# Performance work log

Measured on AMD Instinct MI355X. Metric: run time of the kernel, lower is better.

Reference implementation:

```python
import jax, jax.numpy as jnp
import numpy as np
from math import sqrt

B, L, S, H, E, D = 2, 2048, 2048, 16, 64, 64

def setup_inputs() -> dict:
    key = jax.random.key(0)
    kq, kk, kv = jax.random.split(key, 3)
    queries = jax.random.normal(kq, (B, L, H, E), dtype=jnp.float32)
    keys = jax.random.normal(kk, (B, S, H, E), dtype=jnp.float32)
    values = jax.random.normal(kv, (B, S, H, D), dtype=jnp.float32)
    # causal mask: True where attention is NOT allowed (j > i), matching masked_fill_ semantics
    causal = jnp.triu(jnp.ones((L, S), dtype=jnp.bool_), k=1)
    attn_mask = jnp.broadcast_to(causal[None, None, :, :], (B, 1, L, S))
    return {"queries": queries, "keys": keys, "values": values, "attn_mask": attn_mask}

def reference(queries, keys, values, attn_mask):
    # scores: [B,H,L,S]
    scale = 1.0 / sqrt(queries.shape[-1])
    scores = jnp.einsum('blhe,bshe->bhls', queries, keys)
    scores = jnp.where(attn_mask, -jnp.inf, scores)
    A = jax.nn.softmax(scale * scores, axis=-1)
    V = jnp.einsum('bhls,bshd->blhd', A, values)
    return V
```

## Files before the change

kernel.cpp:

```cpp
#include <hip/hip_runtime.h>

typedef unsigned short ushort_t;
typedef __attribute__((ext_vector_type(8))) short s8v;
typedef __attribute__((ext_vector_type(2))) unsigned u2v;
typedef __attribute__((ext_vector_type(4))) unsigned u4v;
typedef __attribute__((ext_vector_type(4))) float f4;

__device__ __forceinline__ ushort_t f2bf(float x) {
    unsigned u = __builtin_bit_cast(unsigned, x);
    return (ushort_t)((u + 0x7FFFu + ((u >> 16) & 1u)) >> 16);
}
__device__ __forceinline__ unsigned pack_hi16(float lo, float hi) {
    unsigned a = __builtin_bit_cast(unsigned, lo);
    unsigned b = __builtin_bit_cast(unsigned, hi);
    return (a >> 16) | (b & 0xFFFF0000u);
}

__global__ __launch_bounds__(256) void prep_kv(const float* __restrict__ K,
                                               const float* __restrict__ V,
                                               ushort_t* __restrict__ Kb,
                                               ushort_t* __restrict__ VT) {
    __shared__ ushort_t T[64 * 72];
    if (blockIdx.x < 2048) {
        const int gid = blockIdx.x * 256 + threadIdx.x;
        const int e = (gid & 7) * 8;
        const int h = (gid >> 3) & 15;
        const int s = (gid >> 7) & 2047;
        const int b = gid >> 18;
        const float* src = K + (((b * 2048 + s) * 16 + h) * 64 + e);
        f4 a = *(const f4*)src;
        f4 c = *(const f4*)(src + 4);
        s8v o;
        #pragma unroll
        for (int j = 0; j < 4; ++j) { o[j] = (short)f2bf(a[j]); o[j + 4] = (short)f2bf(c[j]); }
        *(s8v*)(Kb + (((b * 16 + h) * 2048 + s) * 64 + e)) = o;
    } else {
        const int v = blockIdx.x - 2048;
        const int s0 = (v & 31) * 64;
        const int h  = (v >> 5) & 15;
        const int b  = v >> 9;
        const int t  = threadIdx.x;
        {
            const int srow = t >> 2, dc = (t & 3) * 16;
            const float* src = V + (((b * 2048 + s0 + srow) * 16 + h) * 64 + dc);
            #pragma unroll
            for (int c = 0; c < 4; ++c) {
                f4 vv = *(const f4*)(src + c * 4);
                #pragma unroll
                for (int j = 0; j < 4; ++j) T[(dc + c * 4 + j) * 72 + srow] = f2bf(vv[j]);
            }
        }
        __syncthreads();
        {
            const int d = t >> 2, sq = (t & 3) * 16;
            ushort_t* dst = VT + (((b * 16 + h) * 64 + d) * 2048 + s0 + sq);
            *(s8v*)(dst)     = *(const s8v*)(&T[d * 72 + sq]);
            *(s8v*)(dst + 8) = *(const s8v*)(&T[d * 72 + sq + 8]);
        }
    }
}

__global__ __launch_bounds__(256, 2) void fattn_main(
    const float* __restrict__ Q,
    const ushort_t* __restrict__ Kb,
    const ushort_t* __restrict__ VTb,
    float* __restrict__ O)
{
    constexpr float K1 = 0.18033688011112042f;
    constexpr float SHIFT = 12.0f;
    __shared__ ushort_t KT0[64 * 72];
    __shared__ ushort_t KT1[64 * 72];
    __shared__ ushort_t VT0[64 * 72];
    __shared__ ushort_t VT1[64 * 72];

    const int bx = blockIdx.x;
    const int bh = bx & 31;
    const int p  = bx >> 5;
    const int b = bh >> 4, h = bh & 15;

    const int wave = threadIdx.x >> 6;
    const int lane = threadIdx.x & 63;
    const int l15  = lane & 15;
    const int quad = lane >> 4;

    const ushort_t* kb  = Kb  + bh * (2048 * 64);
    const ushort_t* vtb = VTb + bh * (64 * 2048);
    const float*    qb  = Q + b * (2048 * 1024) + h * 64;
    float*          ob  = O + b * (2048 * 1024) + h * 64;

    const s8v ones = {0x3F80, 0x3F80, 0x3F80, 0x3F80, 0x3F80, 0x3F80, 0x3F80, 0x3F80};
    const f4 zero4 = {0.f, 0.f, 0.f, 0.f};

    const int sr = threadIdx.x >> 2;
    const int sc = (threadIdx.x & 3) << 4;

    int qr0 = p * 64;

    s8v aq[2];
    f4 oacc[4];
    f4 lsum;

    auto loadQ = [&](int qr) {
        const float* qrow = qb + (qr + wave * 16 + l15) * 1024;
        #pragma unroll
        for (int ks = 0; ks < 2; ++ks) {
            f4 x = *(const f4*)(qrow + ks * 32 + quad * 8);
            f4 y = *(const f4*)(qrow + ks * 32 + quad * 8 + 4);
            #pragma unroll
            for (int j = 0; j < 4; ++j) {
                aq[ks][j]     = (short)f2bf(x[j]);
                aq[ks][j + 4] = (short)f2bf(y[j]);
            }
        }
    };
    auto zeroAcc = [&]() {
        lsum = zero4;
        #pragma unroll
        for (int d = 0; d < 4; ++d) oacc[d] = zero4;
    };
    auto storeO = [&](int qr) {
        #pragma unroll
        for (int r = 0; r < 4; ++r) {
            const float inv = 1.0f / lsum[r];
            const int row = qr + wave * 16 + quad * 4 + r;
            #pragma unroll
            for (int dd = 0; dd < 4; ++dd)
                ob[row * 1024 + dd * 16 + l15] = oacc[dd][r] * inv;
        }
    };

    loadQ(qr0);
    zeroAcc();

    {
        const ushort_t* ksrc = kb + sr * 64 + sc;
        const ushort_t* vsrc = vtb + sr * 2048 + sc;
        s8v k0 = *(const s8v*)(ksrc);
        s8v k1 = *(const s8v*)(ksrc + 8);
        s8v v0 = *(const s8v*)(vsrc);
        s8v v1 = *(const s8v*)(vsrc + 8);
        *(s8v*)&KT0[sr * 72 + sc]     = k0;
        *(s8v*)&KT0[sr * 72 + sc + 8] = k1;
        *(s8v*)&VT0[sr * 72 + sc]     = v0;
        *(s8v*)&VT0[sr * 72 + sc + 8] = v1;
    }
    __syncthreads();

    ushort_t* ktr = KT0;  ushort_t* vtr = VT0;
    ushort_t* ktw = KT1;  ushort_t* vtw = VT1;

    for (int n = 0; n < 33; ++n) {
        s8v gK2[2], gV2[2];
        if (n < 32) {
            const int sn = (n + 1 <= p) ? (n + 1) : (n - p);
            const ushort_t* ksrc = kb + (sn * 64 + sr) * 64 + sc;
            const ushort_t* vsrc = vtb + sr * 2048 + sn * 64 + sc;
            gK2[0] = *(const s8v*)(ksrc);    gK2[1] = *(const s8v*)(ksrc + 8);
            gV2[0] = *(const s8v*)(vsrc);    gV2[1] = *(const s8v*)(vsrc + 8);
        }

        const int s_cur = (n <= p) ? n : (n - p - 1);
        const int n0 = s_cur * 64;
        const bool diag = (n == p) || (n == 32);

        f4 st[4];
        __builtin_amdgcn_s_setprio(1);
        #pragma unroll
        for (int t = 0; t < 4; ++t) {
            const s8v bk0 = *(const s8v*)&ktr[(t * 16 + l15) * 72 + quad * 8];
            const s8v bk1 = *(const s8v*)&ktr[(t * 16 + l15) * 72 + 32 + quad * 8];
            f4 a = __builtin_amdgcn_mfma_f32_16x16x32_bf16(bk0, aq[0], zero4, 0, 0, 0);
            st[t] = __builtin_amdgcn_mfma_f32_16x16x32_bf16(bk1, aq[1], a, 0, 0, 0);
        }
        __builtin_amdgcn_s_setprio(0);

        unsigned w[8];
        #pragma unroll
        for (int t = 0; t < 4; ++t) {
            float pv4[4];
            #pragma unroll
            for (int r = 0; r < 4; ++r) {
                float x = __builtin_fmaf(st[t][r], K1, -SHIFT);
                if (diag) {
                    const int gj = n0 + t * 16 + quad * 4 + r;
                    const int gi = qr0 + wave * 16 + l15;
                    if (gj > gi) x = -INFINITY;
                }
                pv4[r] = __builtin_exp2f(x);
            }
            w[t * 2]     = pack_hi16(pv4[0], pv4[1]);
            w[t * 2 + 1] = pack_hi16(pv4[2], pv4[3]);
        }

        asm volatile("v_permlane32_swap_b32 %0, %1" : "+v"(w[0]), "+v"(w[2]));
        asm volatile("v_permlane32_swap_b32 %0, %1" : "+v"(w[1]), "+v"(w[3]));
        asm volatile("v_permlane32_swap_b32 %0, %1" : "+v"(w[4]), "+v"(w[6]));
        asm volatile("v_permlane32_swap_b32 %0, %1" : "+v"(w[5]), "+v"(w[7]));
        asm volatile("v_permlane16_swap_b32 %0, %1" : "+v"(w[0]), "+v"(w[2]));
        asm volatile("v_permlane16_swap_b32 %0, %1" : "+v"(w[1]), "+v"(w[3]));
        asm volatile("v_permlane16_swap_b32 %0, %1" : "+v"(w[4]), "+v"(w[6]));
        asm volatile("v_permlane16_swap_b32 %0, %1" : "+v"(w[5]), "+v"(w[7]));

        u4v a0v = {w[0], w[1], w[2], w[3]};
        u4v a1v = {w[4], w[5], w[6], w[7]};
        const s8v ap0 = __builtin_bit_cast(s8v, a0v);
        const s8v ap1 = __builtin_bit_cast(s8v, a1v);

        #pragma unroll
        for (int ks = 0; ks < 2; ++ks) {
            s8v bvv[4];
            #pragma unroll
            for (int dd = 0; dd < 4; ++dd)
                bvv[dd] = *(const s8v*)&vtr[(dd * 16 + l15) * 72 + ks * 32 + quad * 8];
            const s8v ap = ks ? ap1 : ap0;
            __builtin_amdgcn_s_setprio(1);
            lsum = __builtin_amdgcn_mfma_f32_16x16x32_bf16(ap, ones, lsum, 0, 0, 0);
            #pragma unroll
            for (int dd = 0; dd < 4; ++dd)
                oacc[dd] = __builtin_amdgcn_mfma_f32_16x16x32_bf16(ap, bvv[dd], oacc[dd], 0, 0, 0);
            __builtin_amdgcn_s_setprio(0);
        }

        if (n < 32) {
            *(s8v*)&ktw[sr * 72 + sc]     = gK2[0];
            *(s8v*)&ktw[sr * 72 + sc + 8] = gK2[1];
            *(s8v*)&vtw[sr * 72 + sc]     = gV2[0];
            *(s8v*)&vtw[sr * 72 + sc + 8] = gV2[1];
        }

        __syncthreads();

        { ushort_t* t0 = ktr; ktr = ktw; ktw = t0; }
        { ushort_t* t1 = vtr; vtr = vtw; vtw = t1; }

        if (n == p) {
            storeO(qr0);
            qr0 = (31 - p) * 64;
            loadQ(qr0);
            zeroAcc();
        }
    }

    storeO(qr0);
}

#define PSTR 72
__global__ __launch_bounds__(256) void fattn_fallback(
    const float* __restrict__ Q, const float* __restrict__ K,
    const float* __restrict__ V, float* __restrict__ O)
{
    constexpr int strL = 1024, strB = 2048 * strL;
    const float scale = 0.125f;
    __shared__ ushort_t KT[64 * PSTR];
    __shared__ ushort_t VT[64 * PSTR];
    __shared__ ushort_t P[4][16 * PSTR];
    const int bh = blockIdx.x & 31;
    const int b = bh >> 4, h = bh & 15;
    const int im = 31 - (blockIdx.x >> 5);
    const int q0 = im * 64;
    const int tid = threadIdx.x, wave = tid >> 6, lane = tid & 63;
    const int l15 = lane & 15, quad = lane >> 4;
    const float* qbase = Q + b*strB + (q0 + wave*16 + l15)*strL + h*64;
    s8v aq0, aq1;
    {
        f4 q0v = *(const f4*)(qbase + quad*8);
        f4 q1v = *(const f4*)(qbase + quad*8 + 4);
        f4 q2v = *(const f4*)(qbase + 32 + quad*8);
        f4 q3v = *(const f4*)(qbase + 32 + quad*8 + 4);
        #pragma unroll
        for (int j = 0; j < 4; ++j) {
            aq0[j] = (short)f2bf(q0v[j]); aq0[j+4] = (short)f2bf(q1v[j]);
            aq1[j] = (short)f2bf(q2v[j]); aq1[j+4] = (short)f2bf(q3v[j]);
        }
    }
    const f4 zero4 = {0.f,0.f,0.f,0.f};
    f4 oacc[4]; float m_prev[4], lsum[4];
    #pragma unroll
    for (int d = 0; d < 4; ++d) oacc[d] = zero4;
    #pragma unroll
    for (int r = 0; r < 4; ++r) { m_prev[r] = -INFINITY; lsum[r] = 0.0f; }
    const float* kh = K + b*strB + h*64;
    const float* vh = V + b*strB + h*64;
    for (int it = 0; it <= im; ++it) {
        const int n0 = it * 64;
        __syncthreads();
        {
            const float* krow = kh + (n0 + lane)*strL + wave*16;
            f4 k0 = *(const f4*)(krow); f4 k1 = *(const f4*)(krow+4);
            f4 k2 = *(const f4*)(krow+8); f4 k3 = *(const f4*)(krow+12);
            s8v kb0, kb1;
            #pragma unroll
            for (int j = 0; j < 4; ++j) {
                kb0[j] = (short)f2bf(k0[j]); kb0[j+4] = (short)f2bf(k1[j]);
                kb1[j] = (short)f2bf(k2[j]); kb1[j+4] = (short)f2bf(k3[j]);
            }
            *(s8v*)&KT[lane*PSTR + wave*16] = kb0;
            *(s8v*)&KT[lane*PSTR + wave*16 + 8] = kb1;
            const float* vrow = vh + (n0 + lane)*strL + wave*16;
            f4 v0 = *(const f4*)(vrow); f4 v1 = *(const f4*)(vrow+4);
            f4 v2 = *(const f4*)(vrow+8); f4 v3 = *(const f4*)(vrow+12);
            #pragma unroll
            for (int j = 0; j < 4; ++j) {
                VT[(wave*16 + j)*PSTR + lane] = f2bf(v0[j]);
                VT[(wave*16 + 4 + j)*PSTR + lane] = f2bf(v1[j]);
                VT[(wave*16 + 8 + j)*PSTR + lane] = f2bf(v2[j]);
                VT[(wave*16 + 12 + j)*PSTR + lane] = f2bf(v3[j]);
            }
        }
        __syncthreads();
        f4 sacc[4];
        #pragma unroll
        for (int t = 0; t < 4; ++t) {
            sacc[t] = zero4;
            const s8v bk0 = *(const s8v*)&KT[(t*16 + l15)*PSTR + quad*8];
            const s8v bk1 = *(const s8v*)&KT[(t*16 + l15)*PSTR + 32 + quad*8];
            sacc[t] = __builtin_amdgcn_mfma_f32_16x16x32_bf16(aq0, bk0, sacc[t], 0, 0, 0);
            sacc[t] = __builtin_amdgcn_mfma_f32_16x16x32_bf16(aq1, bk1, sacc[t], 0, 0, 0);
        }
        const bool diag = (it == im);
        float sv[4][4], rmax[4];
        #pragma unroll
        for (int r = 0; r < 4; ++r) rmax[r] = -INFINITY;
        #pragma unroll
        for (int t = 0; t < 4; ++t)
            #pragma unroll
            for (int r = 0; r < 4; ++r) {
                float x = sacc[t][r] * scale;
                if (diag) {
                    const int gi = wave*16 + quad*4 + r;
                    const int gj = t*16 + l15;
                    if (gj > gi) x = -INFINITY;
                }
                sv[t][r] = x; rmax[r] = fmaxf(rmax[r], x);
            }
        #pragma unroll
        for (int off = 8; off >= 1; off >>= 1)
            #pragma unroll
            for (int r = 0; r < 4; ++r)
                rmax[r] = fmaxf(rmax[r], __shfl_xor(rmax[r], off, 64));
        float mnew[4], alpha[4], rsum[4];
        #pragma unroll
        for (int r = 0; r < 4; ++r) {
            mnew[r] = fmaxf(m_prev[r], rmax[r]);
            alpha[r] = __expf(m_prev[r] - mnew[r]);
            m_prev[r] = mnew[r]; rsum[r] = 0.f;
        }
        #pragma unroll
        for (int t = 0; t < 4; ++t)
            #pragma unroll
            for (int r = 0; r < 4; ++r) {
                const float p = __expf(sv[t][r] - mnew[r]);
                rsum[r] += p;
                P[wave][(quad*4 + r)*PSTR + t*16 + l15] = f2bf(p);
            }
        #pragma unroll
        for (int off = 8; off >= 1; off >>= 1)
            #pragma unroll
            for (int r = 0; r < 4; ++r)
                rsum[r] += __shfl_xor(rsum[r], off, 64);
        #pragma unroll
        for (int r = 0; r < 4; ++r) lsum[r] = alpha[r]*lsum[r] + rsum[r];
        #pragma unroll
        for (int d = 0; d < 4; ++d)
            #pragma unroll
            for (int r = 0; r < 4; ++r) oacc[d][r] *= alpha[r];
        #pragma unroll
        for (int ks = 0; ks < 2; ++ks) {
            const s8v ap = *(const s8v*)&P[wave][l15*PSTR + ks*32 + quad*8];
            #pragma unroll
            for (int d = 0; d < 4; ++d) {
                const s8v bvv = *(const s8v*)&VT[(d*16 + l15)*PSTR + ks*32 + quad*8];
                oacc[d] = __builtin_amdgcn_mfma_f32_16x16x32_bf16(ap, bvv, oacc[d], 0, 0, 0);
            }
        }
    }
    float* obase = O + b*strB + h*64;
    #pragma unroll
    for (int r = 0; r < 4; ++r) {
        const float inv = 1.0f / lsum[r];
        const int gi = q0 + wave*16 + quad*4 + r;
        #pragma unroll
        for (int d = 0; d < 4; ++d)
            obase[gi*strL + d*16 + l15] = oacc[d][r] * inv;
    }
}

extern "C" void kernel_launch(void* const* d_in, const int* in_sizes, int n_in,
                              void* d_out, int out_size, void* d_ws, size_t ws_size,
                              hipStream_t stream) {
    const float* Q = (const float*)d_in[0];
    const float* K = (const float*)d_in[1];
    const float* V = (const float*)d_in[2];
    float* O = (float*)d_out;
    const size_t NEED = 2ull * 4194304ull * 2ull;
    if (ws_size >= NEED) {
        ushort_t* Kb = (ushort_t*)d_ws;
        ushort_t* VT = Kb + 4194304;
        prep_kv<<<3072, 256, 0, stream>>>(K, V, Kb, VT);
        fattn_main<<<512, 256, 0, stream>>>(Q, Kb, VT, O);
    } else {
        fattn_fallback<<<1024, 256, 0, stream>>>(Q, K, V, O);
    }
}
```

Measured before the change: 151.1 us.

## Split causal attention work into balanced blocks with partial-sum combine kernel

Adds a split-KV attention kernel launched with 1024 blocks. Each block pairs a short low query tile with half of a long high query tile's key range, so every block does about 16-17 key-tile iterations. Partial unnormalized outputs and row sums for the high tiles are written to workspace, and a new combine kernel adds the two halves and normalizes them. The goal is to remove causal load imbalance and raise occupancy (launch bounds 4). In exchange it adds a third launch and extra global traffic for the partials.

```diff
diff --git a/kernel.cpp b/kernel.cpp
--- a/kernel.cpp
+++ b/kernel.cpp
@@ -57,6 +57,238 @@
             *(s8v*)(dst)     = *(const s8v*)(&T[d * 72 + sq]);
             *(s8v*)(dst + 8) = *(const s8v*)(&T[d * 72 + sq + 8]);
         }
+    }
+}
+
+__global__ __launch_bounds__(256, 4) void fattn_split(
+    const float* __restrict__ Q,
+    const ushort_t* __restrict__ Kb,
+    const ushort_t* __restrict__ VTb,
+    float* __restrict__ O,
+    float* __restrict__ PP)
+{
+    constexpr float K1 = 0.18033688011112042f;
+    constexpr float SHIFT = 12.0f;
+    __shared__ ushort_t KT0[64 * 72];
+    __shared__ ushort_t KT1[64 * 72];
+    __shared__ ushort_t VT0[64 * 72];
+    __shared__ ushort_t VT1[64 * 72];
+
+    const int bx = blockIdx.x;
+    const int bh = bx & 31;
+    const int slot = bx >> 5;
+    const bool roleA = (slot < 16);
+    const int i = roleA ? slot : (slot - 16);
+    const int tHi = 31 - i;
+    const int NIT = roleA ? 17 : 16;
+    const int b = bh >> 4, h = bh & 15;
+
+    const int wave = threadIdx.x >> 6;
+    const int lane = threadIdx.x & 63;
+    const int l15  = lane & 15;
+    const int quad = lane >> 4;
+
+    const ushort_t* kb  = Kb  + bh * (2048 * 64);
+    const ushort_t* vtb = VTb + bh * (64 * 2048);
+    const float*    qb  = Q + b * (2048 * 1024) + h * 64;
+    float*          ob  = O + b * (2048 * 1024) + h * 64;
+
+    const s8v ones = {0x3F80, 0x3F80, 0x3F80, 0x3F80, 0x3F80, 0x3F80, 0x3F80, 0x3F80};
+    const f4 zero4 = {0.f, 0.f, 0.f, 0.f};
+
+    const int sr = threadIdx.x >> 2;
+    const int sc = (threadIdx.x & 3) << 4;
+
+    auto sTileOf = [&](int n) -> int {
+        return roleA ? ((n <= i) ? n : (n - i - 1)) : (16 - i + n);
+    };
+
+    int qr0 = (roleA ? i : tHi) * 64;
+
+    s8v aq[2];
+    f4 oacc[4];
+    f4 lsum;
+
+    auto loadQ = [&](int qr) {
+        const float* qrow = qb + (qr + wave * 16 + l15) * 1024;
+        #pragma unroll
+        for (int ks = 0; ks < 2; ++ks) {
+            f4 x = *(const f4*)(qrow + ks * 32 + quad * 8);
+            f4 y = *(const f4*)(qrow + ks * 32 + quad * 8 + 4);
+            #pragma unroll
+            for (int j = 0; j < 4; ++j) {
+                aq[ks][j]     = (short)f2bf(x[j]);
+                aq[ks][j + 4] = (short)f2bf(y[j]);
+            }
+        }
+    };
+    auto zeroAcc = [&]() {
+        lsum = zero4;
+        #pragma unroll
+        for (int d = 0; d < 4; ++d) oacc[d] = zero4;
+    };
+    auto storeO = [&](int qr) {
+        #pragma unroll
+        for (int r = 0; r < 4; ++r) {
+            const float inv = 1.0f / lsum[r];
+            const int row = qr + wave * 16 + quad * 4 + r;
+            #pragma unroll
+            for (int dd = 0; dd < 4; ++dd)
+                ob[row * 1024 + dd * 16 + l15] = oacc[dd][r] * inv;
+        }
+    };
+    auto storePartial = [&](int side) {
+        float* base = PP + (size_t)(((side * 32 + bh) * 16 + i) * 4160);
+        #pragma unroll
+        for (int r = 0; r < 4; ++r) {
+            const int rl = wave * 16 + quad * 4 + r;
+            #pragma unroll
+            for (int dd = 0; dd < 4; ++dd)
+                base[rl * 64 + dd * 16 + l15] = oacc[dd][r];
+        }
+        if (l15 == 0) {
+            #pragma unroll
+            for (int r = 0; r < 4; ++r)
+                base[4096 + wave * 16 + quad * 4 + r] = lsum[r];
+        }
+    };
+
+    loadQ(qr0);
+    zeroAcc();
+
+    {
+        const int s0 = sTileOf(0);
+        const ushort_t* ksrc = kb + (s0 * 64 + sr) * 64 + sc;
+        const ushort_t* vsrc = vtb + sr * 2048 + s0 * 64 + sc;
+        s8v k0 = *(const s8v*)(ksrc);
+        s8v k1 = *(const s8v*)(ksrc + 8);
+        s8v v0 = *(const s8v*)(vsrc);
+        s8v v1 = *(const s8v*)(vsrc + 8);
+        *(s8v*)&KT0[sr * 72 + sc]     = k0;
+        *(s8v*)&KT0[sr * 72 + sc + 8] = k1;
+        *(s8v*)&VT0[sr * 72 + sc]     = v0;
+        *(s8v*)&VT0[sr * 72 + sc + 8] = v1;
+    }
+    __syncthreads();
+
+    ushort_t* ktr = KT0;  ushort_t* vtr = VT0;
+    ushort_t* ktw = KT1;  ushort_t* vtw = VT1;
+
+    for (int n = 0; n < NIT; ++n) {
+        s8v gK2[2], gV2[2];
+        if (n + 1 < NIT) {
+            const int sn = sTileOf(n + 1);
+            const ushort_t* ksrc = kb + (sn * 64 + sr) * 64 + sc;
+            const ushort_t* vsrc = vtb + sr * 2048 + sn * 64 + sc;
+            gK2[0] = *(const s8v*)(ksrc);    gK2[1] = *(const s8v*)(ksrc + 8);
+            gV2[0] = *(const s8v*)(vsrc);    gV2[1] = *(const s8v*)(vsrc + 8);
+        }
+
+        const int s_cur = sTileOf(n);
+        const int n0 = s_cur * 64;
+        const bool diag = roleA ? (n == i) : (n == 15);
+
+        f4 st[4];
+        __builtin_amdgcn_s_setprio(1);
+        #pragma unroll
+        for (int t = 0; t < 4; ++t) {
+            const s8v bk0 = *(const s8v*)&ktr[(t * 16 + l15) * 72 + quad * 8];
+            const s8v bk1 = *(const s8v*)&ktr[(t * 16 + l15) * 72 + 32 + quad * 8];
+            f4 a = __builtin_amdgcn_mfma_f32_16x16x32_bf16(bk0, aq[0], zero4, 0, 0, 0);
+            st[t] = __builtin_amdgcn_mfma_f32_16x16x32_bf16(bk1, aq[1], a, 0, 0, 0);
+        }
+        __builtin_amdgcn_s_setprio(0);
+
+        unsigned w[8];
+        #pragma unroll
+        for (int t = 0; t < 4; ++t) {
+            float pv4[4];
+            #pragma unroll
+            for (int r = 0; r < 4; ++r) {
+                float x = __builtin_fmaf(st[t][r], K1, -SHIFT);
+                if (diag) {
+                    const int gj = n0 + t * 16 + quad * 4 + r;
+                    const int gi = qr0 + wave * 16 + l15;
+                    if (gj > gi) x = -INFINITY;
+                }
+                pv4[r] = __builtin_exp2f(x);
+            }
+            w[t * 2]     = pack_hi16(pv4[0], pv4[1]);
+            w[t * 2 + 1] = pack_hi16(pv4[2], pv4[3]);
+        }
+
+        asm volatile("v_permlane32_swap_b32 %0, %1" : "+v"(w[0]), "+v"(w[2]));
+        asm volatile("v_permlane32_swap_b32 %0, %1" : "+v"(w[1]), "+v"(w[3]));
+        asm volatile("v_permlane32_swap_b32 %0, %1" : "+v"(w[4]), "+v"(w[6]));
+        asm volatile("v_permlane32_swap_b32 %0, %1" : "+v"(w[5]), "+v"(w[7]));
+        asm volatile("v_permlane16_swap_b32 %0, %1" : "+v"(w[0]), "+v"(w[2]));
+        asm volatile("v_permlane16_swap_b32 %0, %1" : "+v"(w[1]), "+v"(w[3]));
+        asm volatile("v_permlane16_swap_b32 %0, %1" : "+v"(w[4]), "+v"(w[6]));
+        asm volatile("v_permlane16_swap_b32 %0, %1" : "+v"(w[5]), "+v"(w[7]));
+
+        u4v a0v = {w[0], w[1], w[2], w[3]};
+        u4v a1v = {w[4], w[5], w[6], w[7]};
+        const s8v ap0 = __builtin_bit_cast(s8v, a0v);
+        const s8v ap1 = __builtin_bit_cast(s8v, a1v);
+
+        #pragma unroll
+        for (int ks = 0; ks < 2; ++ks) {
+            s8v bvv[4];
+            #pragma unroll
+            for (int dd = 0; dd < 4; ++dd)
+                bvv[dd] = *(const s8v*)&vtr[(dd * 16 + l15) * 72 + ks * 32 + quad * 8];
+            const s8v ap = ks ? ap1 : ap0;
+            __builtin_amdgcn_s_setprio(1);
+            lsum = __builtin_amdgcn_mfma_f32_16x16x32_bf16(ap, ones, lsum, 0, 0, 0);
+            #pragma unroll
+            for (int dd = 0; dd < 4; ++dd)
+                oacc[dd] = __builtin_amdgcn_mfma_f32_16x16x32_bf16(ap, bvv[dd], oacc[dd], 0, 0, 0);
+            __builtin_amdgcn_s_setprio(0);
+        }
+
+        if (n + 1 < NIT) {
+            *(s8v*)&ktw[sr * 72 + sc]     = gK2[0];
+            *(s8v*)&ktw[sr * 72 + sc + 8] = gK2[1];
+            *(s8v*)&vtw[sr * 72 + sc]     = gV2[0];
+            *(s8v*)&vtw[sr * 72 + sc + 8] = gV2[1];
+        }
+
+        __syncthreads();
+
+        { ushort_t* t0 = ktr; ktr = ktw; ktw = t0; }
+        { ushort_t* t1 = vtr; vtr = vtw; vtw = t1; }
+
+        if (roleA && n == i) {
+            storeO(qr0);
+            qr0 = tHi * 64;
+            loadQ(qr0);
+            zeroAcc();
+        }
+    }
+
+    storePartial(roleA ? 0 : 1);
+}
+
+__global__ __launch_bounds__(256) void combine_split(const float* __restrict__ PP,
+                                                     float* __restrict__ O) {
+    const int blk = blockIdx.x;
+    const int bh = blk >> 4, i = blk & 15;
+    const int b = bh >> 4, h = bh & 15;
+    const float* pa = PP + (size_t)((bh * 16 + i) * 4160);
+    const float* pb = PP + (size_t)(((32 + bh) * 16 + i) * 4160);
+    const int t = threadIdx.x;
+    const int r = t >> 2, c0 = (t & 3) << 4;
+    const float inv = 1.0f / (pa[4096 + r] + pb[4096 + r]);
+    const int grow = (31 - i) * 64 + r;
+    float* orow = O + (size_t)b * 2097152 + (size_t)grow * 1024 + h * 64;
+    #pragma unroll
+    for (int k = 0; k < 4; ++k) {
+        f4 a = *(const f4*)(pa + r * 64 + c0 + k * 4);
+        f4 c = *(const f4*)(pb + r * 64 + c0 + k * 4);
+        f4 o;
+        #pragma unroll
+        for (int j = 0; j < 4; ++j) o[j] = (a[j] + c[j]) * inv;
+        *(f4*)(orow + c0 + k * 4) = o;
     }
 }
 
@@ -392,8 +624,17 @@
     const float* K = (const float*)d_in[1];
     const float* V = (const float*)d_in[2];
     float* O = (float*)d_out;
-    const size_t NEED = 2ull * 4194304ull * 2ull;
-    if (ws_size >= NEED) {
+    const size_t NEED1 = 2ull * 4194304ull * 2ull;
+    const size_t PARTIAL = 2ull * 32ull * 16ull * 4160ull * 4ull;
+    const size_t NEED2 = NEED1 + PARTIAL;
+    if (ws_size >= NEED2) {
+        ushort_t* Kb = (ushort_t*)d_ws;
+        ushort_t* VT = Kb + 4194304;
+        float* PP = (float*)((char*)d_ws + NEED1);
+        prep_kv<<<3072, 256, 0, stream>>>(K, V, Kb, VT);
+        fattn_split<<<1024, 256, 0, stream>>>(Q, Kb, VT, O, PP);
+        combine_split<<<512, 256, 0, stream>>>(PP, O);
+    } else if (ws_size >= NEED1) {
         ushort_t* Kb = (ushort_t*)d_ws;
         ushort_t* VT = Kb + 4194304;
         prep_kv<<<3072, 256, 0, stream>>>(K, V, Kb, VT);
```

New measurement: 154.4 us. +2.2%, slower.
